# Kernel optimization log

Measured on AMD Instinct MI355X. Metric: run time of the kernel, lower is better.

Reference implementation:

```python
import jax, jax.numpy as jnp
import numpy as np

DIM = 1024
H = 16
HD = DIM // H          # head_dim = 64
SCALE = HD ** -0.5
LAMBDA_INIT = 0.1


def setup_inputs() -> dict:
    key = jax.random.key(0)
    ks = jax.random.split(key, 8)
    B, NQ, NKV = 4, 1024, 1024
    # xavier_uniform for linear weights; stored as (in, out) for x @ W
    def xavier(k, fan_in, fan_out):
        a = float(np.sqrt(6.0 / (fan_in + fan_out)))
        return jax.random.uniform(k, (fan_in, fan_out), jnp.float32, -a, a)
    return {
        "DriftData": jax.random.normal(ks[0], (B, NQ, DIM), jnp.float32),
        "OceanData": jax.random.normal(ks[1], (B, NKV, DIM), jnp.float32),
        "Wq": xavier(ks[2], DIM, 2 * DIM),
        "Wk": xavier(ks[3], DIM, 2 * DIM),
        "Wv": xavier(ks[4], DIM, DIM),
        "Wo": xavier(ks[5], DIM, DIM),
        "lambda_q1": jax.random.normal(ks[6], (H, HD), jnp.float32),
        "lambda_k1": jax.random.normal(jax.random.fold_in(ks[6], 1), (H, HD), jnp.float32),
        "lambda_q2": jax.random.normal(ks[7], (H, HD), jnp.float32),
        "lambda_k2": jax.random.normal(jax.random.fold_in(ks[7], 1), (H, HD), jnp.float32),
    }


def reference(DriftData, OceanData, Wq, Wk, Wv, Wo,
              lambda_q1, lambda_k1, lambda_q2, lambda_k2):
    B, NQ, dim = DriftData.shape
    NKV = OceanData.shape[1]
    # lambda scalar per head: exp(q1.k1) - exp(q2.k2) + lambda_init  -> (H,)
    lam = (jnp.exp(jnp.sum(lambda_q1 * lambda_k1, axis=-1))
           - jnp.exp(jnp.sum(lambda_q2 * lambda_k2, axis=-1)) + LAMBDA_INIT)
    # projections: Q,K -> 2*dim, V -> dim
    Q = (DriftData @ Wq).reshape(B, NQ, H, 2 * HD).transpose(0, 2, 1, 3)   # b h q 2hd
    K = (OceanData @ Wk).reshape(B, NKV, H, 2 * HD).transpose(0, 2, 1, 3)  # b h k 2hd
    V = (OceanData @ Wv).reshape(B, NKV, H, HD).transpose(0, 2, 1, 3)      # b h k hd
    Q1, Q2 = Q[..., :HD], Q[..., HD:]
    K1, K2 = K[..., :HD], K[..., HD:]
    A1 = jnp.einsum('bhqd,bhkd->bhqk', Q1, K1) * SCALE
    A2 = jnp.einsum('bhqd,bhkd->bhqk', Q2, K2) * SCALE
    att = jax.nn.softmax(A1, axis=-1) - lam[None, :, None, None] * jax.nn.softmax(A2, axis=-1)
    out = jnp.einsum('bhqk,bhkd->bhqd', att, V)            # b h q hd
    out = out.transpose(0, 2, 1, 3).reshape(B, NQ, dim)    # b q dim
    return out @ Wo
```

## Files before the change

### kernel.cpp

```cpp
#include <hip/hip_runtime.h>
#include <hip/hip_bf16.h>

typedef unsigned short u16;
typedef unsigned int u32;
typedef __attribute__((ext_vector_type(8))) short short8;
typedef __attribute__((ext_vector_type(4))) float f32x4;
typedef __attribute__((ext_vector_type(4))) u16 us4;

#define MFMA16(a,b,c) __builtin_amdgcn_mfma_f32_16x16x32_bf16(a,b,c,0,0,0)

__device__ __forceinline__ u16 f2b(float x){
  u32 u = __builtin_bit_cast(u32, x);
  u32 r = (u + 0x7fffu + ((u >> 16) & 1u)) >> 16;
  return (u16)r;
}
__device__ __forceinline__ u16 f2b_hw(float x){
  return __builtin_bit_cast(u16, __float2bfloat16(x));
}
__device__ __forceinline__ float ex2(float x){ return __builtin_amdgcn_exp2f(x); }
__device__ __forceinline__ float b2f(u16 v){ return __builtin_bit_cast(float, ((u32)v) << 16); }

__device__ __forceinline__ void gll16(const u16* g, u16* l){
  __builtin_amdgcn_global_load_lds((const __attribute__((address_space(1))) u32*)g,
                                   (__attribute__((address_space(3))) u32*)l, 16, 0, 0);
}

__global__ __launch_bounds__(256) void k_prep(const float* __restrict__ Drift, const float* __restrict__ Ocean,
                                              const float* __restrict__ Wq, const float* __restrict__ Wk,
                                              const float* __restrict__ Wv, const float* __restrict__ Wo,
                                              u16* __restrict__ Xd, u16* __restrict__ Xo,
                                              u16* __restrict__ WqT, u16* __restrict__ WkvT,
                                              u16* __restrict__ WoT,
                                              const float* __restrict__ lq1, const float* __restrict__ lk1,
                                              const float* __restrict__ lq2, const float* __restrict__ lk2,
                                              float* __restrict__ lam){
  __shared__ float t[32][33];
  int bid = blockIdx.x;
  if (bid < 8192){
    const float* x = (bid < 4096) ? Drift : Ocean;
    u16* y = (bid < 4096) ? Xd : Xo;
    int i = (bid & 4095) * 256 + threadIdx.x;
    float4 v = reinterpret_cast<const float4*>(x)[i];
    us4 o; o.x = f2b(v.x); o.y = f2b(v.y); o.z = f2b(v.z); o.w = f2b(v.w);
    reinterpret_cast<us4*>(y)[i] = o;
    return;
  }
  int tt = bid - 8192;
  int z = tt >> 11;
  int bx = tt & 63, by = (tt & 2047) >> 6;
  const float* W; u16* WT; int N; float scale = 1.0f;
  if (z == 0){ W = Wq; WT = WqT; N = 2048; scale = 0.1803368867f; }
  else if (z == 1){ W = Wk; WT = WkvT; N = 2048; }
  else if (z == 2){ W = Wv; WT = WkvT + 2048*1024; N = 1024; }
  else { W = Wo; WT = WoT; N = 1024; }
  int n0 = bx * 32, k0 = by * 32;
  int tx = threadIdx.x & 31, ty = threadIdx.x >> 5;
  if (n0 < N){
    #pragma unroll
    for (int i = 0; i < 4; i++)
      t[ty + i*8][tx] = W[(size_t)(k0 + ty + i*8) * N + n0 + tx];
    __syncthreads();
    #pragma unroll
    for (int i = 0; i < 4; i++)
      WT[(size_t)(n0 + ty + i*8) * 1024 + k0 + tx] = f2b(t[tx][ty + i*8] * scale);
  }
  if (z == 3 && bx == 0 && by == 0 && threadIdx.x < 16){
    int h = threadIdx.x;
    float d1 = 0.f, d2 = 0.f;
    for (int i = 0; i < 64; i++){
      d1 += lq1[h*64 + i] * lk1[h*64 + i];
      d2 += lq2[h*64 + i] * lk2[h*64 + i];
    }
    lam[h] = expf(d1) - expf(d2) + 0.1f;
  }
}

__global__ __launch_bounds__(256) void k_transpose_v(const u16* __restrict__ KV, u16* __restrict__ VT){
  __shared__ u16 t[32][34];
  int kv0 = blockIdx.x * 32, d0 = blockIdx.y * 32, bh = blockIdx.z;
  int b = bh >> 4, h = bh & 15;
  int tx = threadIdx.x & 31, ty = threadIdx.x >> 5;
  #pragma unroll
  for (int i = 0; i < 4; i++)
    t[ty + i*8][tx] = KV[(size_t)(b*1024 + kv0 + ty + i*8) * 3072 + 2048 + h*64 + d0 + tx];
  __syncthreads();
  #pragma unroll
  for (int i = 0; i < 4; i++)
    VT[(size_t)bh * 65536 + (size_t)(d0 + ty + i*8) * 1024 + kv0 + tx] = t[tx][ty + i*8];
}

template<bool OUTF32>
__device__ __forceinline__ void gemm_body(const u16* __restrict__ A, const u16* __restrict__ B,
                                          void* __restrict__ C, int N, int m0, int n0,
                                          u16* As, u16* Bs){
  const int tid = threadIdx.x;
  const int wave = tid >> 6, lane = tid & 63;
  const int lr = lane & 15, lg = lane >> 4;
  const int wm = wave >> 1, wn = wave & 1;

  f32x4 acc[4][4];
  #pragma unroll
  for (int i = 0; i < 4; i++)
    #pragma unroll
    for (int j = 0; j < 4; j++){ f32x4 z = {0.f,0.f,0.f,0.f}; acc[i][j] = z; }

  const int srow = tid >> 3;
  const int skc  = tid & 7;

  for (int k0 = 0; k0 < 1024; k0 += 64){
    #pragma unroll
    for (int c = 0; c < 4; c++){
      int row = c*32 + srow;
      const u16* ga = A + (size_t)(m0 + row) * 1024 + k0 + ((skc ^ (row & 7)) << 3);
      gll16(ga, As + c*2048 + wave*512);
      const u16* gb = B + (size_t)(n0 + row) * 1024 + k0 + ((skc ^ (row & 7)) << 3);
      gll16(gb, Bs + c*2048 + wave*512);
    }
    __syncthreads();
    #pragma unroll
    for (int kc = 0; kc < 2; kc++){
      short8 af[4], bfr[4];
      #pragma unroll
      for (int mt = 0; mt < 4; mt++){
        int row = wm*64 + mt*16 + lr;
        af[mt] = *reinterpret_cast<const short8*>(As + row*64 + (((kc*4 + lg) ^ (row & 7)) << 3));
      }
      #pragma unroll
      for (int nt = 0; nt < 4; nt++){
        int rown = wn*64 + nt*16 + lr;
        bfr[nt] = *reinterpret_cast<const short8*>(Bs + rown*64 + (((kc*4 + lg) ^ (rown & 7)) << 3));
      }
      #pragma unroll
      for (int mt = 0; mt < 4; mt++)
        #pragma unroll
        for (int nt = 0; nt < 4; nt++)
          acc[mt][nt] = MFMA16(af[mt], bfr[nt], acc[mt][nt]);
    }
    __syncthreads();
  }
  #pragma unroll
  for (int mt = 0; mt < 4; mt++)
    #pragma unroll
    for (int nt = 0; nt < 4; nt++)
      #pragma unroll
      for (int r = 0; r < 4; r++){
        int row = m0 + wm*64 + mt*16 + lg*4 + r;
        int col = n0 + wn*64 + nt*16 + lr;
        if (OUTF32) ((float*)C)[(size_t)row * N + col] = acc[mt][nt][r];
        else        ((u16*)C)[(size_t)row * N + col] = f2b(acc[mt][nt][r]);
      }
}

__global__ __launch_bounds__(256) void k_gemm_proj(const u16* __restrict__ Xd, const u16* __restrict__ Xo,
                                                   const u16* __restrict__ WqT, const u16* __restrict__ WkvT,
                                                   u16* __restrict__ Qb, u16* __restrict__ KVb){
  __shared__ __align__(16) u16 As[128*64];
  __shared__ __align__(16) u16 Bs[128*64];
  int bid0 = blockIdx.x;
  int bid = (bid0 & 7) * 160 + (bid0 >> 3);
  if (bid < 512){
    gemm_body<false>(Xd, WqT, Qb, 2048, (bid >> 4) * 128, (bid & 15) * 128, As, Bs);
  } else {
    int t = bid - 512;
    gemm_body<false>(Xo, WkvT, KVb, 3072, (t / 24) * 128, (t % 24) * 128, As, Bs);
  }
}

__global__ __launch_bounds__(256) void k_gemm_out(const u16* __restrict__ A, const u16* __restrict__ B,
                                                  float* __restrict__ C){
  __shared__ __align__(16) u16 As[128*64];
  __shared__ __align__(16) u16 Bs[128*64];
  int bid = blockIdx.x;
  gemm_body<true>(A, B, C, 1024, (bid >> 3) * 128, (bid & 7) * 128, As, Bs);
}

__device__ __forceinline__ void softmax_t(f32x4 s[4], float& l, u16* pl, int lr, int lg, int swzv){
  float sum = 0.f;
  #pragma unroll
  for (int nt = 0; nt < 4; nt++)
    #pragma unroll
    for (int r = 0; r < 4; r++){
      float p = ex2(s[nt][r]);
      s[nt][r] = p;
      sum += p;
    }
  sum += __shfl_xor(sum, 16);
  sum += __shfl_xor(sum, 32);
  l += sum;
  char* base = (char*)pl + lr * 128;
  #pragma unroll
  for (int nt = 0; nt < 4; nt++){
    us4 h;
    h.x = f2b_hw(s[nt][0]); h.y = f2b_hw(s[nt][1]);
    h.z = f2b_hw(s[nt][2]); h.w = f2b_hw(s[nt][3]);
    *reinterpret_cast<us4*>(base + ((nt*32 + lg*8) ^ (swzv << 4))) = h;
  }
}

__global__ __launch_bounds__(512) void k_attn(const u16* __restrict__ Q, const u16* __restrict__ KVb,
                                              const u16* __restrict__ VT, const float* __restrict__ lam,
                                              u16* __restrict__ O){
  int bid = blockIdx.x;
  int logical = (bid & 7) * 32 + (bid >> 3);
  int qt2 = logical & 3, h = (logical >> 2) & 15, b = logical >> 6;
  const int tid = threadIdx.x, wave = tid >> 6, lane = tid & 63;
  const int lr = lane & 15, lg = lane >> 4;
  const int br = wave >> 2, wq = wave & 3;
  const int swzv = (lr ^ (lr >> 3)) & 7;

  __shared__ __align__(16) u16 Ks[3][8192];
  __shared__ __align__(16) u16 Vs[3][4096];
  __shared__ __align__(16) u16 Pl[8][4][1024];

  const int srow = tid >> 4, schunk = tid & 15;
  const int vrow = tid >> 3, vchunk = tid & 7;
  const u16* Kg = KVb + (size_t)(b*1024 + srow) * 3072 + h*128 + ((schunk ^ (srow & 7)) << 3);
  const u16* Vg = VT + (size_t)(b*16 + h) * 65536 + (size_t)vrow * 1024 + ((vchunk ^ (vrow & 7)) << 3);

  short8 qf[4][2];
  #pragma unroll
  for (int qt = 0; qt < 4; qt++){
    const u16* Qp = Q + (size_t)(b*1024 + qt2*256 + wq*64 + qt*16 + lr) * 2048 + h*128 + br*64 + lg*8;
    qf[qt][0] = *reinterpret_cast<const short8*>(Qp);
    qf[qt][1] = *reinterpret_cast<const short8*>(Qp + 32);
  }
  const float lamh = lam[h];

  f32x4 o[4][4];
  #pragma unroll
  for (int nt = 0; nt < 4; nt++)
    #pragma unroll
    for (int qt = 0; qt < 4; qt++){ f32x4 z = {0.f,0.f,0.f,0.f}; o[nt][qt] = z; }
  float l[4] = {0.f, 0.f, 0.f, 0.f};

  auto STAGE = [&](int buf, int kv0){
    #pragma unroll
    for (int i = 0; i < 2; i++)
      gll16(Kg + (size_t)(kv0 + i*32) * 3072, &Ks[buf][i*4096 + tid*8]);
    gll16(Vg + kv0, &Vs[buf][tid*8]);
  };

  STAGE(0, 0);
  STAGE(1, 64);
  asm volatile("s_waitcnt vmcnt(3)" ::: "memory");
  __builtin_amdgcn_s_barrier();
  __builtin_amdgcn_sched_barrier(0);

  u16* Plw = &Pl[wave][0][0];

  for (int t = 0; t < 16; t++){
    const int cur = t % 3;
    if (t <= 13) STAGE((t + 2) % 3, (t + 2) << 6);

    const u16* kbuf = &Ks[cur][0];
    const u16* vbuf = &Vs[cur][0];

    short8 kf[4][2];
    #pragma unroll
    for (int nt = 0; nt < 4; nt++)
      #pragma unroll
      for (int kc = 0; kc < 2; kc++)
        kf[nt][kc] = *reinterpret_cast<const short8*>(
            kbuf + (nt*16 + lr)*128 + (((br*8 + kc*4 + lg) ^ (lr & 7)) << 3));
    #pragma unroll
    for (int qt = 0; qt < 4; qt++){
      f32x4 s[4];
      #pragma unroll
      for (int nt = 0; nt < 4; nt++){ f32x4 z = {0.f,0.f,0.f,0.f}; s[nt] = z; }
      __builtin_amdgcn_s_setprio(1);
      #pragma unroll
      for (int nt = 0; nt < 4; nt++)
        #pragma unroll
        for (int kc = 0; kc < 2; kc++)
          s[nt] = MFMA16(kf[nt][kc], qf[qt][kc], s[nt]);
      __builtin_amdgcn_s_setprio(0);
      softmax_t(s, l[qt], Plw + qt*1024, lr, lg, swzv);
    }

    #pragma unroll
    for (int kc = 0; kc < 2; kc++){
      short8 pf[4];
      #pragma unroll
      for (int qt = 0; qt < 4; qt++)
        pf[qt] = *reinterpret_cast<const short8*>(
            (char*)(Plw + qt*1024) + lr*128 + ((kc*64 + lg*16) ^ (swzv << 4)));
      __builtin_amdgcn_s_setprio(1);
      #pragma unroll
      for (int nt = 0; nt < 4; nt++){
        short8 vf = *reinterpret_cast<const short8*>(
            vbuf + (nt*16 + lr)*64 + (((kc*4 + lg) ^ (lr & 7)) << 3));
        #pragma unroll
        for (int qt = 0; qt < 4; qt++)
          o[nt][qt] = MFMA16(vf, pf[qt], o[nt][qt]);
      }
      __builtin_amdgcn_s_setprio(0);
    }

    if (t <= 13){
      asm volatile("s_waitcnt vmcnt(3)" ::: "memory");
      __builtin_amdgcn_s_barrier();
      __builtin_amdgcn_sched_barrier(0);
    } else if (t == 14){
      asm volatile("s_waitcnt vmcnt(0)" ::: "memory");
      __builtin_amdgcn_s_barrier();
      __builtin_amdgcn_sched_barrier(0);
    }
  }

  if (br == 1){
    #pragma unroll
    for (int qt = 0; qt < 4; qt++){
      const float inv2 = lamh / l[qt];
      char* base = (char*)(Plw + qt*1024) + lr * 128;
      #pragma unroll
      for (int nt = 0; nt < 4; nt++){
        us4 hh;
        #pragma unroll
        for (int r = 0; r < 4; r++)
          ((u16*)&hh)[r] = f2b_hw(o[nt][qt][r] * inv2);
        *reinterpret_cast<us4*>(base + ((nt*32 + lg*8) ^ (swzv << 4))) = hh;
      }
    }
  }
  __syncthreads();
  if (br == 0){
    u16* Px = &Pl[wave + 4][0][0];
    #pragma unroll
    for (int qt = 0; qt < 4; qt++){
      const float inv1 = 1.0f / l[qt];
      char* base = (char*)(Px + qt*1024) + lr * 128;
      u16* Op = O + (size_t)(b*1024 + qt2*256 + wq*64 + qt*16 + lr) * 1024 + h*64;
      #pragma unroll
      for (int nt = 0; nt < 4; nt++){
        us4 x = *reinterpret_cast<const us4*>(base + ((nt*32 + lg*8) ^ (swzv << 4)));
        us4 hh;
        #pragma unroll
        for (int r = 0; r < 4; r++){
          float v = o[nt][qt][r] * inv1 - b2f(((const u16*)&x)[r]);
          ((u16*)&hh)[r] = f2b_hw(v);
        }
        *reinterpret_cast<us4*>(Op + nt*16 + lg*4) = hh;
      }
    }
  }
}

extern "C" void kernel_launch(void* const* d_in, const int* in_sizes, int n_in,
                              void* d_out, int out_size, void* d_ws, size_t ws_size,
                              hipStream_t stream){
  const float* Drift = (const float*)d_in[0];
  const float* Ocean = (const float*)d_in[1];
  const float* Wq    = (const float*)d_in[2];
  const float* Wk    = (const float*)d_in[3];
  const float* Wv    = (const float*)d_in[4];
  const float* Wo    = (const float*)d_in[5];
  const float* lq1   = (const float*)d_in[6];
  const float* lk1   = (const float*)d_in[7];
  const float* lq2   = (const float*)d_in[8];
  const float* lk2   = (const float*)d_in[9];
  float* out = (float*)d_out;

  char* ws = (char*)d_ws;
  u16* Xd   = (u16*)(ws);
  u16* Xo   = (u16*)(ws + 8388608);
  u16* WqT  = (u16*)(ws + 16777216);
  u16* WkvT = (u16*)(ws + 20971520);
  u16* WoT  = (u16*)(ws + 27262976);
  u16* Qb   = (u16*)(ws + 29360128);
  u16* KVb  = (u16*)(ws + 46137344);
  u16* VTb  = (u16*)(ws + 71303168);
  u16* Ob   = (u16*)(ws + 79691776);
  float* lam = (float*)(ws + 88080384);

  k_prep<<<16384, 256, 0, stream>>>(Drift, Ocean, Wq, Wk, Wv, Wo, Xd, Xo,
                                    WqT, WkvT, WoT, lq1, lk1, lq2, lk2, lam);
  k_gemm_proj<<<1280, 256, 0, stream>>>(Xd, Xo, WqT, WkvT, Qb, KVb);
  k_transpose_v<<<dim3(32,2,64), 256, 0, stream>>>(KVb, VTb);
  k_attn<<<256, 512, 0, stream>>>(Qb, KVb, VTb, lam, Ob);
  k_gemm_out<<<256, 256, 0, stream>>>(Ob, WoT, out);
}
```

Baseline: 141.6 us.

## Compute V transposed inside projection GEMM and double-buffer GEMM LDS staging

Drops the separate V transpose kernel. The projection GEMM now produces V already transposed by computing Wv^T·Xo^T with swapped operands, writing a (head_dim, batch*kv) layout that the attention kernel reads directly. K is stored in its own buffer with a 2048 stride. The shared GEMM body now double-buffers its LDS tiles, raises wave priority around the MFMA block, and uses hardware bf16 conversion. Oddly, the proj kernel launches 512 threads but half exit immediately, which may hurt occupancy. The doubled LDS footprint may also reduce blocks per CU.

```diff
diff --git a/kernel.cpp b/kernel.cpp
--- a/kernel.cpp
+++ b/kernel.cpp
@@ -75,20 +75,6 @@
   }
 }
 
-__global__ __launch_bounds__(256) void k_transpose_v(const u16* __restrict__ KV, u16* __restrict__ VT){
-  __shared__ u16 t[32][34];
-  int kv0 = blockIdx.x * 32, d0 = blockIdx.y * 32, bh = blockIdx.z;
-  int b = bh >> 4, h = bh & 15;
-  int tx = threadIdx.x & 31, ty = threadIdx.x >> 5;
-  #pragma unroll
-  for (int i = 0; i < 4; i++)
-    t[ty + i*8][tx] = KV[(size_t)(b*1024 + kv0 + ty + i*8) * 3072 + 2048 + h*64 + d0 + tx];
-  __syncthreads();
-  #pragma unroll
-  for (int i = 0; i < 4; i++)
-    VT[(size_t)bh * 65536 + (size_t)(d0 + ty + i*8) * 1024 + kv0 + tx] = t[tx][ty + i*8];
-}
-
 template<bool OUTF32>
 __device__ __forceinline__ void gemm_body(const u16* __restrict__ A, const u16* __restrict__ B,
                                           void* __restrict__ C, int N, int m0, int n0,
@@ -97,6 +83,7 @@
   const int wave = tid >> 6, lane = tid & 63;
   const int lr = lane & 15, lg = lane >> 4;
   const int wm = wave >> 1, wn = wave & 1;
+  const int srow = tid >> 3, skc = tid & 7;
 
   f32x4 acc[4][4];
   #pragma unroll
@@ -104,39 +91,54 @@
     #pragma unroll
     for (int j = 0; j < 4; j++){ f32x4 z = {0.f,0.f,0.f,0.f}; acc[i][j] = z; }
 
-  const int srow = tid >> 3;
-  const int skc  = tid & 7;
-
-  for (int k0 = 0; k0 < 1024; k0 += 64){
+  auto STAGE = [&](int buf, int k0){
     #pragma unroll
     for (int c = 0; c < 4; c++){
       int row = c*32 + srow;
       const u16* ga = A + (size_t)(m0 + row) * 1024 + k0 + ((skc ^ (row & 7)) << 3);
-      gll16(ga, As + c*2048 + wave*512);
+      gll16(ga, As + buf*8192 + c*2048 + wave*512);
       const u16* gb = B + (size_t)(n0 + row) * 1024 + k0 + ((skc ^ (row & 7)) << 3);
-      gll16(gb, Bs + c*2048 + wave*512);
-    }
-    __syncthreads();
+      gll16(gb, Bs + buf*8192 + c*2048 + wave*512);
+    }
+  };
+
+  STAGE(0, 0);
+  asm volatile("s_waitcnt vmcnt(0)" ::: "memory");
+  __builtin_amdgcn_s_barrier();
+  __builtin_amdgcn_sched_barrier(0);
+
+  for (int t = 0; t < 16; t++){
+    const int cur = t & 1;
+    if (t < 15) STAGE(cur ^ 1, (t + 1) << 6);
+
+    const u16* as = As + cur*8192;
+    const u16* bs = Bs + cur*8192;
     #pragma unroll
     for (int kc = 0; kc < 2; kc++){
       short8 af[4], bfr[4];
       #pragma unroll
       for (int mt = 0; mt < 4; mt++){
         int row = wm*64 + mt*16 + lr;
-        af[mt] = *reinterpret_cast<const short8*>(As + row*64 + (((kc*4 + lg) ^ (row & 7)) << 3));
+        af[mt] = *reinterpret_cast<const short8*>(as + row*64 + (((kc*4 + lg) ^ (row & 7)) << 3));
       }
       #pragma unroll
       for (int nt = 0; nt < 4; nt++){
         int rown = wn*64 + nt*16 + lr;
-        bfr[nt] = *reinterpret_cast<const short8*>(Bs + rown*64 + (((kc*4 + lg) ^ (rown & 7)) << 3));
-      }
+        bfr[nt] = *reinterpret_cast<const short8*>(bs + rown*64 + (((kc*4 + lg) ^ (rown & 7)) << 3));
+      }
+      __builtin_amdgcn_s_setprio(1);
       #pragma unroll
       for (int mt = 0; mt < 4; mt++)
         #pragma unroll
         for (int nt = 0; nt < 4; nt++)
           acc[mt][nt] = MFMA16(af[mt], bfr[nt], acc[mt][nt]);
-    }
-    __syncthreads();
+      __builtin_amdgcn_s_setprio(0);
+    }
+    if (t < 15){
+      asm volatile("s_waitcnt vmcnt(0)" ::: "memory");
+      __builtin_amdgcn_s_barrier();
+      __builtin_amdgcn_sched_barrier(0);
+    }
   }
   #pragma unroll
   for (int mt = 0; mt < 4; mt++)
@@ -147,29 +149,34 @@
         int row = m0 + wm*64 + mt*16 + lg*4 + r;
         int col = n0 + wn*64 + nt*16 + lr;
         if (OUTF32) ((float*)C)[(size_t)row * N + col] = acc[mt][nt][r];
-        else        ((u16*)C)[(size_t)row * N + col] = f2b(acc[mt][nt][r]);
-      }
-}
-
-__global__ __launch_bounds__(256) void k_gemm_proj(const u16* __restrict__ Xd, const u16* __restrict__ Xo,
+        else        ((u16*)C)[(size_t)row * N + col] = f2b_hw(acc[mt][nt][r]);
+      }
+}
+
+__global__ __launch_bounds__(512) void k_gemm_proj(const u16* __restrict__ Xd, const u16* __restrict__ Xo,
                                                    const u16* __restrict__ WqT, const u16* __restrict__ WkvT,
-                                                   u16* __restrict__ Qb, u16* __restrict__ KVb){
-  __shared__ __align__(16) u16 As[128*64];
-  __shared__ __align__(16) u16 Bs[128*64];
+                                                   u16* __restrict__ Qb, u16* __restrict__ Kb,
+                                                   u16* __restrict__ VTb){
+  __shared__ __align__(16) u16 As[2*8192];
+  __shared__ __align__(16) u16 Bs[2*8192];
+  if (threadIdx.x >= 256) return;
   int bid0 = blockIdx.x;
   int bid = (bid0 & 7) * 160 + (bid0 >> 3);
   if (bid < 512){
     gemm_body<false>(Xd, WqT, Qb, 2048, (bid >> 4) * 128, (bid & 15) * 128, As, Bs);
+  } else if (bid < 1024){
+    int t = bid - 512;
+    gemm_body<false>(Xo, WkvT, Kb, 2048, (t >> 4) * 128, (t & 15) * 128, As, Bs);
   } else {
-    int t = bid - 512;
-    gemm_body<false>(Xo, WkvT, KVb, 3072, (t / 24) * 128, (t % 24) * 128, As, Bs);
+    int t = bid - 1024;
+    gemm_body<false>(WkvT + 2048*1024, Xo, VTb, 4096, (t >> 5) * 128, (t & 31) * 128, As, Bs);
   }
 }
 
 __global__ __launch_bounds__(256) void k_gemm_out(const u16* __restrict__ A, const u16* __restrict__ B,
                                                   float* __restrict__ C){
-  __shared__ __align__(16) u16 As[128*64];
-  __shared__ __align__(16) u16 Bs[128*64];
+  __shared__ __align__(16) u16 As[2*8192];
+  __shared__ __align__(16) u16 Bs[2*8192];
   int bid = blockIdx.x;
   gemm_body<true>(A, B, C, 1024, (bid >> 3) * 128, (bid & 7) * 128, As, Bs);
 }
@@ -197,7 +204,7 @@
   }
 }
 
-__global__ __launch_bounds__(512) void k_attn(const u16* __restrict__ Q, const u16* __restrict__ KVb,
+__global__ __launch_bounds__(512) void k_attn(const u16* __restrict__ Q, const u16* __restrict__ Kb,
                                               const u16* __restrict__ VT, const float* __restrict__ lam,
                                               u16* __restrict__ O){
   int bid = blockIdx.x;
@@ -214,8 +221,8 @@
 
   const int srow = tid >> 4, schunk = tid & 15;
   const int vrow = tid >> 3, vchunk = tid & 7;
-  const u16* Kg = KVb + (size_t)(b*1024 + srow) * 3072 + h*128 + ((schunk ^ (srow & 7)) << 3);
-  const u16* Vg = VT + (size_t)(b*16 + h) * 65536 + (size_t)vrow * 1024 + ((vchunk ^ (vrow & 7)) << 3);
+  const u16* Kg = Kb + (size_t)(b*1024 + srow) * 2048 + h*128 + ((schunk ^ (srow & 7)) << 3);
+  const u16* Vg = VT + (size_t)(h*64 + vrow) * 4096 + b*1024 + ((vchunk ^ (vrow & 7)) << 3);
 
   short8 qf[4][2];
   #pragma unroll
@@ -236,7 +243,7 @@
   auto STAGE = [&](int buf, int kv0){
     #pragma unroll
     for (int i = 0; i < 2; i++)
-      gll16(Kg + (size_t)(kv0 + i*32) * 3072, &Ks[buf][i*4096 + tid*8]);
+      gll16(Kg + (size_t)(kv0 + i*32) * 2048, &Ks[buf][i*4096 + tid*8]);
     gll16(Vg + kv0, &Vs[buf][tid*8]);
   };
 
@@ -367,15 +374,14 @@
   u16* WkvT = (u16*)(ws + 20971520);
   u16* WoT  = (u16*)(ws + 27262976);
   u16* Qb   = (u16*)(ws + 29360128);
-  u16* KVb  = (u16*)(ws + 46137344);
+  u16* Kb   = (u16*)(ws + 46137344);
   u16* VTb  = (u16*)(ws + 71303168);
   u16* Ob   = (u16*)(ws + 79691776);
   float* lam = (float*)(ws + 88080384);
 
   k_prep<<<16384, 256, 0, stream>>>(Drift, Ocean, Wq, Wk, Wv, Wo, Xd, Xo,
                                     WqT, WkvT, WoT, lq1, lk1, lq2, lk2, lam);
-  k_gemm_proj<<<1280, 256, 0, stream>>>(Xd, Xo, WqT, WkvT, Qb, KVb);
-  k_transpose_v<<<dim3(32,2,64), 256, 0, stream>>>(KVb, VTb);
-  k_attn<<<256, 512, 0, stream>>>(Qb, KVb, VTb, lam, Ob);
+  k_gemm_proj<<<1280, 512, 0, stream>>>(Xd, Xo, WqT, WkvT, Qb, Kb, VTb);
+  k_attn<<<256, 512, 0, stream>>>(Qb, Kb, VTb, lam, Ob);
   k_gemm_out<<<256, 256, 0, stream>>>(Ob, WoT, out);
 }
```

Result: no change. 143.3 us (+1.2%).

## Triple-buffer GEMM LDS tiles with async prefetch two stages ahead

Applied to the files above, without the earlier changes.

The shared GEMM body (used by the projection and output GEMMs) now keeps three LDS buffers and issues global-to-LDS loads for tile t+2 while computing tile t. Partial vmcnt waits with a single barrier per iteration replace the two full __syncthreads per k-step. s_setprio is raised around the MFMA block. LDS use per block triples to 96 KB, which can lower occupancy. An unused dead lambda (STAGE) is left in.

```diff
diff --git a/kernel.cpp b/kernel.cpp
--- a/kernel.cpp
+++ b/kernel.cpp
@@ -97,6 +97,7 @@
   const int wave = tid >> 6, lane = tid & 63;
   const int lr = lane & 15, lg = lane >> 4;
   const int wm = wave >> 1, wn = wave & 1;
+  const int srow = tid >> 3, skc = tid & 7;
 
   f32x4 acc[4][4];
   #pragma unroll
@@ -104,39 +105,72 @@
     #pragma unroll
     for (int j = 0; j < 4; j++){ f32x4 z = {0.f,0.f,0.f,0.f}; acc[i][j] = z; }
 
-  const int srow = tid >> 3;
-  const int skc  = tid & 7;
-
-  for (int k0 = 0; k0 < 1024; k0 += 64){
+  auto STAGE = [&](int buf, int t){
+    const int k0 = t << 6;
     #pragma unroll
     for (int c = 0; c < 4; c++){
       int row = c*32 + srow;
       const u16* ga = A + (size_t)(m0 + row) * 1024 + k0 + ((skc ^ (row & 7)) << 3);
-      gll16(ga, As + c*2048 + wave*512);
+      gll16(ga, As + buf*4096 + c*1024 + wave*256 + (tid & 63)*0 + (tid - wave*64)*0 + ( (tid & 63) * 8 ) - ((tid & 63) * 8) + ( ( (tid & 63) ) * 8 ));
+    }
+  };
+  (void)STAGE;
+
+  auto STAGE2 = [&](int buf, int t){
+    const int k0 = t << 6;
+    #pragma unroll
+    for (int c = 0; c < 4; c++){
+      int row = c*32 + srow;
+      const u16* ga = A + (size_t)(m0 + row) * 1024 + k0 + ((skc ^ (row & 7)) << 3);
+      gll16(ga, As + buf*8192 + c*2048 + wave*512);
       const u16* gb = B + (size_t)(n0 + row) * 1024 + k0 + ((skc ^ (row & 7)) << 3);
-      gll16(gb, Bs + c*2048 + wave*512);
-    }
-    __syncthreads();
+      gll16(gb, Bs + buf*8192 + c*2048 + wave*512);
+    }
+  };
+
+  STAGE2(0, 0);
+  STAGE2(1, 1);
+  asm volatile("s_waitcnt vmcnt(8)" ::: "memory");
+  __builtin_amdgcn_s_barrier();
+  __builtin_amdgcn_sched_barrier(0);
+
+  for (int t = 0; t < 16; t++){
+    const int cur = t % 3;
+    if (t <= 13) STAGE2((t + 2) % 3, t + 2);
+
+    const u16* as = As + cur*8192;
+    const u16* bs = Bs + cur*8192;
     #pragma unroll
     for (int kc = 0; kc < 2; kc++){
       short8 af[4], bfr[4];
       #pragma unroll
       for (int mt = 0; mt < 4; mt++){
         int row = wm*64 + mt*16 + lr;
-        af[mt] = *reinterpret_cast<const short8*>(As + row*64 + (((kc*4 + lg) ^ (row & 7)) << 3));
+        af[mt] = *reinterpret_cast<const short8*>(as + row*64 + (((kc*4 + lg) ^ (row & 7)) << 3));
       }
       #pragma unroll
       for (int nt = 0; nt < 4; nt++){
         int rown = wn*64 + nt*16 + lr;
-        bfr[nt] = *reinterpret_cast<const short8*>(Bs + rown*64 + (((kc*4 + lg) ^ (rown & 7)) << 3));
-      }
+        bfr[nt] = *reinterpret_cast<const short8*>(bs + rown*64 + (((kc*4 + lg) ^ (rown & 7)) << 3));
+      }
+      __builtin_amdgcn_s_setprio(1);
       #pragma unroll
       for (int mt = 0; mt < 4; mt++)
         #pragma unroll
         for (int nt = 0; nt < 4; nt++)
           acc[mt][nt] = MFMA16(af[mt], bfr[nt], acc[mt][nt]);
-    }
-    __syncthreads();
+      __builtin_amdgcn_s_setprio(0);
+    }
+
+    if (t <= 13){
+      asm volatile("s_waitcnt vmcnt(8)" ::: "memory");
+      __builtin_amdgcn_s_barrier();
+      __builtin_amdgcn_sched_barrier(0);
+    } else if (t == 14){
+      asm volatile("s_waitcnt vmcnt(0)" ::: "memory");
+      __builtin_amdgcn_s_barrier();
+      __builtin_amdgcn_sched_barrier(0);
+    }
   }
   #pragma unroll
   for (int mt = 0; mt < 4; mt++)
@@ -154,8 +188,8 @@
 __global__ __launch_bounds__(256) void k_gemm_proj(const u16* __restrict__ Xd, const u16* __restrict__ Xo,
                                                    const u16* __restrict__ WqT, const u16* __restrict__ WkvT,
                                                    u16* __restrict__ Qb, u16* __restrict__ KVb){
-  __shared__ __align__(16) u16 As[128*64];
-  __shared__ __align__(16) u16 Bs[128*64];
+  __shared__ __align__(16) u16 As[3*8192];
+  __shared__ __align__(16) u16 Bs[3*8192];
   int bid0 = blockIdx.x;
   int bid = (bid0 & 7) * 160 + (bid0 >> 3);
   if (bid < 512){
@@ -168,8 +202,8 @@
 
 __global__ __launch_bounds__(256) void k_gemm_out(const u16* __restrict__ A, const u16* __restrict__ B,
                                                   float* __restrict__ C){
-  __shared__ __align__(16) u16 As[128*64];
-  __shared__ __align__(16) u16 Bs[128*64];
+  __shared__ __align__(16) u16 As[3*8192];
+  __shared__ __align__(16) u16 Bs[3*8192];
   int bid = blockIdx.x;
   gemm_body<true>(A, B, C, 1024, (bid >> 3) * 128, (bid & 7) * 128, As, Bs);
 }
```

After: 178.9 us. 1.26x slower.
